# Kernel optimization log

Hardware: AMD Instinct MI355X
Metric: run time of the kernel (lower is better)

The kernel has to match this reference:

```python
import jax, jax.numpy as jnp
import numpy as np
from jax.scipy.special import gammaln

S, N, T = 8, 32, 262144
EPS = 1e-16  # emission clamp, as in torch .clamp(min=1e-16)


def setup_inputs() -> dict:
    key = jax.random.key(0)
    k1, k2, k3, k4 = jax.random.split(key, 4)
    spikes = jax.random.randint(k1, (T, N), 0, 2).astype(jnp.int32)  # binary counts
    convolved_spikes = 0.5 * jax.random.normal(k2, (T, N), dtype=jnp.float32)
    weight = 0.1 * jax.random.normal(k3, (S, N, N), dtype=jnp.float32)
    bias = 0.1 * jax.random.normal(k4, (N,), dtype=jnp.float32)
    eye = jnp.eye(S, dtype=jnp.float32)
    transition_matrix = eye * 0.98 + (0.02 / (S - 1)) * (1.0 - eye)
    return {"spikes": spikes, "convolved_spikes": convolved_spikes,
            "weight": weight, "bias": bias, "transition_matrix": transition_matrix}


def reference(spikes, convolved_spikes, weight, bias, transition_matrix):
    n_states = weight.shape[0]
    init_p = jnp.ones(n_states, dtype=convolved_spikes.dtype) / n_states
    A = transition_matrix  # (S, S)

    # firing_rates: sigmoid(bias + conv @ W[s].T) -> (S, T, N)
    rates = jax.nn.sigmoid(bias[None, None, :] +
                           jnp.einsum('tn,smn->stm', convolved_spikes, weight))
    x = spikes.astype(rates.dtype)
    # Poisson log-likelihood summed over neurons, then (S,T) -> (T,S)
    log_emission = (x[None] * jnp.log(rates) - rates - gammaln(x + 1.0)[None]).sum(-1).T

    emission = jnp.clip(jnp.exp(log_emission), EPS)  # (T, S)

    # forward pass (scaling)
    a0 = init_p * emission[0]
    c0 = a0.sum()
    a0 = a0 / c0

    def fstep(a_prev, em_t):
        a = em_t * (A.T @ a_prev)
        c = a.sum()
        an = a / c
        return an, (an, c)

    _, (alpha_rest, c_rest) = jax.lax.scan(fstep, a0, emission[1:])
    alpha = jnp.concatenate([a0[None], alpha_rest])  # (T, S)
    c = jnp.concatenate([c0[None], c_rest])          # (T,)

    # backward pass
    def bstep(b_next, ec):
        em_t1, c_t1 = ec
        b = A @ (b_next * em_t1) / c_t1
        return b, b

    b_last = jnp.ones(n_states, dtype=emission.dtype)
    _, beta_head = jax.lax.scan(bstep, b_last, (emission[1:], c[1:]), reverse=True)
    beta = jnp.concatenate([beta_head, b_last[None]])  # (T, S)

    gamma = alpha * beta  # (T, S)
    xi = (alpha[:-1, :, None] * emission[1:, None, :] *
          A[None, :, :] * beta[1:, None, :]) / c[1:, None, None]  # (T-1, S, S)
    return gamma, xi
```

## Files before the change

### kernel.cpp

```cpp
#include <hip/hip_runtime.h>
#include <math.h>


constexpr int TT  = 262144;
constexpr int LL  = 64;
constexpr int CK  = TT / LL;
constexpr int CPG = 16;
constexpr int NG  = CK / CPG;
constexpr int NSG = 16;
constexpr int EP  = 516;

typedef __attribute__((ext_vector_type(8))) short bf16x8;
typedef __attribute__((ext_vector_type(4))) float f32x4;

__device__ __forceinline__ float rcp_nr(float x) {
  float r = __builtin_amdgcn_rcpf(x);
  return r * (2.0f - x * r);
}
__device__ __forceinline__ unsigned short f2bf(float f) {
  unsigned u = __float_as_uint(f);
  u += 0x7FFFu + ((u >> 16) & 1u);
  return (unsigned short)(u >> 16);
}
__device__ __forceinline__ float bf2f(unsigned short h) {
  return __uint_as_float(((unsigned)h) << 16);
}

#define SWZ8(x, k) __int_as_float(__builtin_amdgcn_ds_swizzle(__float_as_int(x), (((k) << 5) | 0x18)))
#define SWZX(x, d) __int_as_float(__builtin_amdgcn_ds_swizzle(__float_as_int(x), (((d) << 10) | 0x1F)))
#define BPERM(a, x) __int_as_float(__builtin_amdgcn_ds_bpermute((a), __float_as_int(x)))

#define TREE8(dst, v) { float s01=v[0]+v[1], s23=v[2]+v[3], s45=v[4]+v[5], s67=v[6]+v[7]; dst = (s01+s23)+(s45+s67); }

__global__ __launch_bounds__(256) void k_emission(
    const int* __restrict__ spikes, const float* __restrict__ conv,
    const float* __restrict__ W, const float* __restrict__ bias,
    float* __restrict__ em, float* __restrict__ iemax) {
  __shared__ short sWbf[256 * 40];
  __shared__ unsigned sMask[64];
  const int tid = threadIdx.x;
  const int lane = tid & 63;
  const int wv = tid >> 6;
  const int T0 = blockIdx.x * 64;
  const int q = lane & 15;
  const int rg = lane >> 4;

#pragma unroll
  for (int it = 0; it < 8; ++it) {
    int idx4 = tid + it * 256;
    float4 w4 = ((const float4*)W)[idx4];
    int sm = idx4 >> 3, n0 = (idx4 & 7) << 2;
    ushort4 h;
    h.x = f2bf(w4.x); h.y = f2bf(w4.y); h.z = f2bf(w4.z); h.w = f2bf(w4.w);
    *(ushort4*)&sWbf[sm * 40 + n0] = h;
  }
#pragma unroll
  for (int it = 0; it < 8; ++it) {
    int idx = it * 256 + tid;
    int t = idx >> 5;
    int v = spikes[(size_t)(T0 + t) * 32 + (idx & 31)];
    unsigned long long b = __ballot(v != 0);
    if ((lane & 31) == 0) sMask[t] = (unsigned)(b >> (lane & 32));
  }
  __syncthreads();

  const int tg0 = T0 + wv * 16;
  const float* cp = conv + (size_t)(tg0 + q) * 32 + rg * 8;
  float4 ca = *(const float4*)cp;
  float4 cb = *(const float4*)(cp + 4);
  bf16x8 ch, cl;
  {
    float cv[8] = {ca.x, ca.y, ca.z, ca.w, cb.x, cb.y, cb.z, cb.w};
#pragma unroll
    for (int e2 = 0; e2 < 8; ++e2) {
      unsigned short hb = f2bf(cv[e2]);
      ch[e2] = (short)hb;
      cl[e2] = (short)f2bf(cv[e2] - bf2f(hb));
    }
  }
  const float4 bjlo = ((const float4*)bias)[rg];
  const float4 bjhi = ((const float4*)bias)[rg + 4];
  const unsigned mk = sMask[wv * 16 + q];
  constexpr float L2E = 1.4426950408889634f;
  const f32x4 zacc = {0.f, 0.f, 0.f, 0.f};

  float les[8];
#pragma unroll
  for (int s = 0; s < 8; ++s) {
    float part0 = 0.f, part1 = 0.f;
#pragma unroll
    for (int par = 0; par < 2; ++par) {
      const int tile = s * 2 + par;
      bf16x8 wf = *(bf16x8*)&sWbf[(tile * 16 + q) * 40 + rg * 8];
      f32x4 acc = __builtin_amdgcn_mfma_f32_16x16x32_bf16(wf, cl, zacc, 0, 0, 0);
      acc = __builtin_amdgcn_mfma_f32_16x16x32_bf16(wf, ch, acc, 0, 0, 0);
      const float4 bj = par ? bjhi : bjlo;
      float bja[4] = {bj.x, bj.y, bj.z, bj.w};
      float sumr = 0.f, pr = 1.f;
#pragma unroll
      for (int r = 0; r < 4; ++r) {
        float z = acc[r] + bja[r];
        float u = __builtin_amdgcn_exp2f(z * -L2E);
        float p = 1.f + u;
        sumr += __builtin_amdgcn_rcpf(p);
        int m = par * 16 + rg * 4 + r;
        pr *= ((mk >> m) & 1u) ? p : 1.f;
      }
      sumr += SWZX(sumr, 16); sumr += __shfl_xor(sumr, 32);
      pr   *= SWZX(pr, 16);   pr   *= __shfl_xor(pr, 32);
      float pt = fmaf(-L2E, sumr, -__builtin_amdgcn_logf(pr));
      if (par == 0) part0 = pt; else part1 = pt;
    }
    les[s] = part0 + part1;
  }
  float e[8];
#pragma unroll
  for (int s = 0; s < 8; ++s) e[s] = fmaxf(__builtin_amdgcn_exp2f(les[s]), 1e-16f);
  float mx = e[0];
#pragma unroll
  for (int s = 1; s < 8; ++s) mx = fmaxf(mx, e[s]);
  if (lane < 16) {
    float4 o0 = {e[0], e[1], e[2], e[3]};
    float4 o1 = {e[4], e[5], e[6], e[7]};
    *(float4*)&em[(size_t)(tg0 + q) * 8] = o0;
    *(float4*)&em[(size_t)(tg0 + q) * 8 + 4] = o1;
    iemax[tg0 + q] = rcp_nr(mx);
  }
}

__global__ __launch_bounds__(128) void k_fwd_chunks(
    const float* __restrict__ em, const float* __restrict__ iemax,
    const float* __restrict__ A, float* __restrict__ Pf,
    float* __restrict__ Gf) {
  __shared__ float sE[16 * EP];
  __shared__ float sM[16 * 64];
  const int tid = threadIdx.x;
  const int cl = tid >> 3, jc = tid & 7;
  const int c = blockIdx.x * 16 + cl;
  const float b_ = A[1];
  const float aa = A[0] - b_;

  for (int idx = tid; idx < 8192; idx += 128) {
    int gi = blockIdx.x * 8192 + idx;
    sE[(idx >> 9) * EP + (idx & 511)] = em[gi] * iemax[gi >> 3];
  }
  __syncthreads();

  float p[8];
#pragma unroll
  for (int k = 0; k < 8; ++k) p[k] = (k == jc) ? 1.f : 0.f;
  const float* eb = &sE[cl * EP];
  for (int t = 0; t < 64; ++t) {
    float4 e0 = *(const float4*)&eb[t * 8];
    float4 e1 = *(const float4*)&eb[t * 8 + 4];
    float e[8] = {e0.x, e0.y, e0.z, e0.w, e1.x, e1.y, e1.z, e1.w};
    if (c == 0 && t == 0) {
#pragma unroll
      for (int r = 0; r < 8; ++r) p[r] = e[r] * p[r];
    } else {
      float sg; TREE8(sg, p);
      float bs = b_ * sg;
#pragma unroll
      for (int r = 0; r < 8; ++r) p[r] = e[r] * fmaf(aa, p[r], bs);
    }
    if ((t & 7) == 7) {
      float m = p[0];
#pragma unroll
      for (int k = 1; k < 8; ++k) m = fmaxf(m, p[k]);
      m = fmaxf(m, SWZX(m, 1)); m = fmaxf(m, SWZX(m, 2)); m = fmaxf(m, SWZX(m, 4));
      float rm = __builtin_amdgcn_rcpf(m);
#pragma unroll
      for (int k = 0; k < 8; ++k) p[k] *= rm;
    }
  }
#pragma unroll
  for (int r = 0; r < 8; ++r) {
    sM[cl * 64 + r * 8 + jc] = p[r];
    Pf[(size_t)c * 64 + r * 8 + jc] = p[r];
  }
  __syncthreads();

  if (tid < 64) {
    const int L = tid;
    int ad[8];
#pragma unroll
    for (int k = 0; k < 8; ++k) ad[k] = (((k << 3) | (L & 7))) << 2;
    float S = sM[L];
    for (int m = 1; m < 16; ++m) {
      float4 r0 = *(const float4*)&sM[m * 64 + (L >> 3) * 8];
      float4 r1 = *(const float4*)&sM[m * 64 + (L >> 3) * 8 + 4];
      float acc;
      acc =      r0.x * BPERM(ad[0], S);
      acc = fmaf(r0.y,  BPERM(ad[1], S), acc);
      acc = fmaf(r0.z,  BPERM(ad[2], S), acc);
      acc = fmaf(r0.w,  BPERM(ad[3], S), acc);
      acc = fmaf(r1.x,  BPERM(ad[4], S), acc);
      acc = fmaf(r1.y,  BPERM(ad[5], S), acc);
      acc = fmaf(r1.z,  BPERM(ad[6], S), acc);
      acc = fmaf(r1.w,  BPERM(ad[7], S), acc);
      S = acc;
      if ((m & 3) == 3) {
        float mx = S;
        mx = fmaxf(mx, SWZX(mx, 1));  mx = fmaxf(mx, SWZX(mx, 2));
        mx = fmaxf(mx, SWZX(mx, 4));  mx = fmaxf(mx, SWZX(mx, 8));
        mx = fmaxf(mx, SWZX(mx, 16)); mx = fmaxf(mx, __shfl_xor(mx, 32));
        S *= __builtin_amdgcn_rcpf(mx);
      }
    }
    Gf[(size_t)blockIdx.x * 64 + L] = S;
  }
}

__global__ __launch_bounds__(1024) void k_fwd_mid(
    const float* __restrict__ Gf, float* __restrict__ vg) {
  __shared__ float sG[NG * 64];
  __shared__ float sgS[NSG * 64];
  __shared__ float sgE[NSG * 8];
  const int tid = threadIdx.x, wv = tid >> 6, L = tid & 63;
  for (int idx = tid; idx < NG * 64; idx += 1024) sG[idx] = Gf[idx];
  __syncthreads();

  int ad[8];
#pragma unroll
  for (int k = 0; k < 8; ++k) ad[k] = (((k << 3) | (L & 7))) << 2;
  const int ad2 = ((L & 7) * 9) << 2;

  {
    float S = sG[wv * 1024 + L];
    for (int m = 1; m < 16; ++m) {
      const float* mb = &sG[(wv * 16 + m) * 64 + (L >> 3) * 8];
      float4 r0 = *(const float4*)mb;
      float4 r1 = *(const float4*)(mb + 4);
      float acc;
      acc =      r0.x * BPERM(ad[0], S);
      acc = fmaf(r0.y,  BPERM(ad[1], S), acc);
      acc = fmaf(r0.z,  BPERM(ad[2], S), acc);
      acc = fmaf(r0.w,  BPERM(ad[3], S), acc);
      acc = fmaf(r1.x,  BPERM(ad[4], S), acc);
      acc = fmaf(r1.y,  BPERM(ad[5], S), acc);
      acc = fmaf(r1.z,  BPERM(ad[6], S), acc);
      acc = fmaf(r1.w,  BPERM(ad[7], S), acc);
      S = acc;
      if ((m & 3) == 3) {
        float mx = S;
        mx = fmaxf(mx, SWZX(mx, 1));  mx = fmaxf(mx, SWZX(mx, 2));
        mx = fmaxf(mx, SWZX(mx, 4));  mx = fmaxf(mx, SWZX(mx, 8));
        mx = fmaxf(mx, SWZX(mx, 16)); mx = fmaxf(mx, __shfl_xor(mx, 32));
        S *= __builtin_amdgcn_rcpf(mx);
      }
    }
    sgS[wv * 64 + L] = S;
  }
  __syncthreads();

  if (wv == 0) {
    float vj = 0.125f;
    for (int sg = 0; sg < 16; ++sg) {
      if (L < 8) sgE[sg * 8 + L] = vj;
      float t = sgS[sg * 64 + L] * vj;
      t += SWZX(t, 1); t += SWZX(t, 2); t += SWZX(t, 4);
      float t2 = t + SWZX(t, 8); t2 += SWZX(t2, 16); t2 += __shfl_xor(t2, 32);
      vj = BPERM(ad2, t) * rcp_nr(t2);
    }
  }
  __syncthreads();

  {
    float vj = sgE[wv * 8 + (L & 7)];
    for (int gl = 0; gl < 16; ++gl) {
      int g = wv * 16 + gl;
      if (L < 8) vg[g * 8 + L] = vj;
      float t = sG[g * 64 + L] * vj;
      t += SWZX(t, 1); t += SWZX(t, 2); t += SWZX(t, 4);
      float t2 = t + SWZX(t, 8); t2 += SWZX(t2, 16); t2 += __shfl_xor(t2, 32);
      vj = BPERM(ad2, t) * rcp_nr(t2);
    }
  }
}

__global__ __launch_bounds__(128) void k_fwd_replay(
    const float* __restrict__ em, const float* __restrict__ A,
    const float* __restrict__ Pf, const float* __restrict__ vg,
    float* __restrict__ bf, float* __restrict__ alpha,
    float* __restrict__ cvec) {
  __shared__ float sE[16 * EP];
  __shared__ float sBf[16 * 8];
  const int tid = threadIdx.x;
  const int cl = tid >> 3, jl = tid & 7;
  const int c = blockIdx.x * 16 + cl;
  const float b_ = A[1];
  const float aa = A[0] - b_;

  for (int idx = tid; idx < 8192; idx += 128)
    sE[(idx >> 9) * EP + (idx & 511)] = em[(size_t)blockIdx.x * 8192 + idx];

  if (tid < 64) {
    const int L = tid;
    const int ad2 = ((L & 7) * 9) << 2;
    float f[16];
#pragma unroll
    for (int m = 0; m < 16; ++m) f[m] = Pf[(size_t)(blockIdx.x * 16 + m) * 64 + L];
    float vj = vg[blockIdx.x * 8 + (L & 7)];
#pragma unroll
    for (int m = 0; m < 16; ++m) {
      if (L < 8) {
        sBf[m * 8 + L] = vj;
        bf[(size_t)(blockIdx.x * 16 + m) * 8 + L] = vj;
      }
      float t = f[m] * vj;
      t += SWZX(t, 1); t += SWZX(t, 2); t += SWZX(t, 4);
      float t2 = t + SWZX(t, 8); t2 += SWZX(t2, 16); t2 += __shfl_xor(t2, 32);
      vj = BPERM(ad2, t) * rcp_nr(t2);
    }
  }
  __syncthreads();

  float u[8];
#pragma unroll
  for (int k = 0; k < 8; ++k) u[k] = sBf[cl * 8 + k];
  float rs = 1.f;
  const float* eb = &sE[cl * EP];
  for (int t = 0; t < 64; ++t) {
    float4 e0 = *(const float4*)&eb[t * 8];
    float4 e1 = *(const float4*)&eb[t * 8 + 4];
    float e[8] = {e0.x, e0.y, e0.z, e0.w, e1.x, e1.y, e1.z, e1.w};
    float un[8];
    if (c == 0 && t == 0) {
#pragma unroll
      for (int r = 0; r < 8; ++r) un[r] = 0.125f * e[r];
    } else {
      float sg; TREE8(sg, u);
      float bs = b_ * sg;
#pragma unroll
      for (int r = 0; r < 8; ++r) un[r] = (e[r] * rs) * fmaf(aa, u[r], bs);
    }
    float s; TREE8(s, un);
    float rsn = rcp_nr(s);
    float myu = un[0];
#pragma unroll
    for (int k = 1; k < 8; ++k) myu = (jl == k) ? un[k] : myu;
    int tg = c * 64 + t;
    alpha[(size_t)tg * 8 + jl] = myu * rsn;
    if (jl == 0) cvec[tg] = s;
#pragma unroll
    for (int k = 0; k < 8; ++k) u[k] = un[k];
    rs = rsn;
  }
}

__global__ __launch_bounds__(128) void k_bwd_chunks(
    const float* __restrict__ em, const float* __restrict__ cvec,
    const float* __restrict__ A, float* __restrict__ Rb,
    float* __restrict__ Gb) {
  __shared__ float sS[16 * EP];
  __shared__ float sM[16 * 64];
  const int tid = threadIdx.x;
  const int cl = tid >> 3, il = tid & 7;
  const int c = blockIdx.x * 16 + cl;
  const float b_ = A[1];
  const float aa = A[0] - b_;

  for (int idx = tid; idx < 8192; idx += 128) {
    int gi = blockIdx.x * 8192 + idx;
    sS[(idx >> 9) * EP + (idx & 511)] = em[gi] * rcp_nr(cvec[gi >> 3]);
  }
  __syncthreads();

  float rv[8];
#pragma unroll
  for (int k = 0; k < 8; ++k) rv[k] = (k == il) ? 1.f : 0.f;
  const float* db = &sS[cl * EP];
  for (int t = 0; t < 64; ++t) {
    float4 d0 = *(const float4*)&db[t * 8];
    float4 d1 = *(const float4*)&db[t * 8 + 4];
    float d[8] = {d0.x, d0.y, d0.z, d0.w, d1.x, d1.y, d1.z, d1.w};
    float sg; TREE8(sg, rv);
    float bs = b_ * sg;
#pragma unroll
    for (int j = 0; j < 8; ++j) rv[j] = fmaf(aa, rv[j], bs) * d[j];
  }
  {
    float4 o0 = {rv[0], rv[1], rv[2], rv[3]};
    float4 o1 = {rv[4], rv[5], rv[6], rv[7]};
    *(float4*)&sM[cl * 64 + il * 8] = o0;
    *(float4*)&sM[cl * 64 + il * 8 + 4] = o1;
    *(float4*)&Rb[(size_t)c * 64 + il * 8] = o0;
    *(float4*)&Rb[(size_t)c * 64 + il * 8 + 4] = o1;
  }
  __syncthreads();

  if (tid < 64) {
    const int L = tid;
    float S = sM[L];
    for (int m = 1; m < 16; ++m) {
      const float* mb = &sM[m * 64 + (L & 7)];
      float acc;
      acc =      SWZ8(S, 0) * mb[0];
      acc = fmaf(SWZ8(S, 1), mb[8],  acc);
      acc = fmaf(SWZ8(S, 2), mb[16], acc);
      acc = fmaf(SWZ8(S, 3), mb[24], acc);
      acc = fmaf(SWZ8(S, 4), mb[32], acc);
      acc = fmaf(SWZ8(S, 5), mb[40], acc);
      acc = fmaf(SWZ8(S, 6), mb[48], acc);
      acc = fmaf(SWZ8(S, 7), mb[56], acc);
      S = acc;
    }
    Gb[(size_t)blockIdx.x * 64 + L] = S;
  }
}

__global__ __launch_bounds__(1024) void k_bwd_mid(
    const float* __restrict__ Gb, float* __restrict__ wg) {
  __shared__ float sG[NG * 64];
  __shared__ float sgS[NSG * 64];
  __shared__ float sgE[NSG * 8];
  const int tid = threadIdx.x, wv = tid >> 6, L = tid & 63;
  for (int idx = tid; idx < NG * 64; idx += 1024) sG[idx] = Gb[idx];
  __syncthreads();

  const int ad2 = ((L & 7) * 9) << 2;
  {
    float S = sG[wv * 1024 + L];
    for (int m = 1; m < 16; ++m) {
      const float* mb = &sG[(wv * 16 + m) * 64 + (L & 7)];
      float acc;
      acc =      SWZ8(S, 0) * mb[0];
      acc = fmaf(SWZ8(S, 1), mb[8],  acc);
      acc = fmaf(SWZ8(S, 2), mb[16], acc);
      acc = fmaf(SWZ8(S, 3), mb[24], acc);
      acc = fmaf(SWZ8(S, 4), mb[32], acc);
      acc = fmaf(SWZ8(S, 5), mb[40], acc);
      acc = fmaf(SWZ8(S, 6), mb[48], acc);
      acc = fmaf(SWZ8(S, 7), mb[56], acc);
      S = acc;
    }
    sgS[wv * 64 + L] = S;
  }
  __syncthreads();

  if (wv == 0) {
    float wj = 1.f;
    for (int sg = 15; sg >= 0; --sg) {
      if (L < 8) sgE[sg * 8 + L] = wj;
      float t = sgS[sg * 64 + L] * wj;
      t += SWZX(t, 1); t += SWZX(t, 2); t += SWZX(t, 4);
      wj = BPERM(ad2, t);
    }
  }
  __syncthreads();

  {
    float wj = sgE[wv * 8 + (L & 7)];
    for (int gl = 15; gl >= 0; --gl) {
      int g = wv * 16 + gl;
      if (L < 8) wg[g * 8 + L] = wj;
      float t = sG[g * 64 + L] * wj;
      t += SWZX(t, 1); t += SWZX(t, 2); t += SWZX(t, 4);
      wj = BPERM(ad2, t);
    }
  }
}

__global__ __launch_bounds__(1024) void k_bwd_replay(
    const float* __restrict__ em, const float* __restrict__ cvec,
    const float* __restrict__ A, const float* __restrict__ bf,
    const float* __restrict__ wg, const float* __restrict__ Rb,
    float* __restrict__ gamma, float* __restrict__ xi) {
  __shared__ float sQ[16 * 512];
  __shared__ float sAl[16 * 512];
  __shared__ float sGb[16 * 8];
  const int tid = threadIdx.x, wv = tid >> 6, L = tid & 63;
  const int i = L >> 3, j = L & 7;
  const int c = blockIdx.x * 16 + wv;
  const float Aij = A[i * 8 + j];

  for (int idx = tid; idx < 8192; idx += 1024) {
    int gi = blockIdx.x * 8192 + idx;
    sQ[idx] = em[gi] * rcp_nr(cvec[gi >> 3]);
    int cl2 = idx >> 9, rr = (idx >> 3) & 63, s = idx & 7;
    float av;
    if (rr == 0) av = bf[(blockIdx.x * 16 + cl2) * 8 + s];
    else av = gamma[((size_t)(blockIdx.x * 16 + cl2) * 64 + rr - 1) * 8 + s];
    sAl[idx] = av;
  }
  if (wv == 0) {
    const int ad2 = ((L & 7) * 9) << 2;
    float f[16];
#pragma unroll
    for (int m = 0; m < 16; ++m) f[m] = Rb[(size_t)(blockIdx.x * 16 + m) * 64 + L];
    float vj = wg[blockIdx.x * 8 + (L & 7)];
#pragma unroll
    for (int m = 15; m >= 0; --m) {
      if (L < 8) sGb[m * 8 + L] = vj;
      float t = f[m] * vj;
      t += SWZX(t, 1); t += SWZX(t, 2); t += SWZX(t, 4);
      vj = BPERM(ad2, t);
    }
  }
  __syncthreads();

  float b = sGb[wv * 8 + j];
  {
    int te = c * 64 + 63;
    if (L < 8) {
      float al = gamma[(size_t)te * 8 + L];
      gamma[(size_t)te * 8 + L] = al * b;
    }
  }
  for (int t = 63; t >= 0; --t) {
    int tg = c * 64 + t;
    float q = sQ[wv * 512 + t * 8 + j] * b;
    float apv = sAl[wv * 512 + t * 8 + i];
    if (tg > 0) xi[(size_t)(tg - 1) * 64 + L] = apv * Aij * q;
    float p = Aij * q;
    p += SWZX(p, 1); p += SWZX(p, 2); p += SWZX(p, 4);
    if (t > 0 && j == 0) gamma[(size_t)(tg - 1) * 8 + i] = apv * p;
    b = __shfl(p, (L & 7) * 8);
  }
}

extern "C" void kernel_launch(void* const* d_in, const int* in_sizes, int n_in,
                              void* d_out, int out_size, void* d_ws, size_t ws_size,
                              hipStream_t stream) {
  const int*   spikes = (const int*)  d_in[0];
  const float* conv   = (const float*)d_in[1];
  const float* W      = (const float*)d_in[2];
  const float* bias   = (const float*)d_in[3];
  const float* A      = (const float*)d_in[4];

  float* out   = (float*)d_out;
  float* gamma = out;
  float* xi    = out + (size_t)TT * 8;

  float* ws    = (float*)d_ws;
  float* em    = ws;
  float* iemax = em + (size_t)TT * 8;
  float* cvec  = iemax + TT;
  float* Pf    = cvec + TT;
  float* Rb    = Pf;
  float* Gf    = Pf + (size_t)CK * 64;
  float* Gb    = Gf;
  float* vg    = Gf + NG * 64;
  float* wg    = vg + NG * 8;
  float* bf    = wg + NG * 8;
  (void)in_sizes; (void)n_in; (void)out_size; (void)ws_size;

  k_emission  <<<TT / 64, 256, 0, stream>>>(spikes, conv, W, bias, em, iemax);
  k_fwd_chunks<<<NG, 128, 0, stream>>>(em, iemax, A, Pf, Gf);
  k_fwd_mid   <<<1, 1024, 0, stream>>>(Gf, vg);
  k_fwd_replay<<<NG, 128, 0, stream>>>(em, A, Pf, vg, bf, gamma, cvec);
  k_bwd_chunks<<<NG, 128, 0, stream>>>(em, cvec, A, Rb, Gb);
  k_bwd_mid   <<<1, 1024, 0, stream>>>(Gb, wg);
  k_bwd_replay<<<NG, 1024, 0, stream>>>(em, cvec, A, bf, wg, Rb, gamma, xi);
}
```

Before: 143.3 us.

## Fuse forward replay with backward chunk pass and restructure emission MFMA loop

Merges the forward replay kernel and the backward chunk-transfer kernel into one launch. It reuses the emission tile already in shared memory and keeps the per-step reciprocal scaling constants in LDS, so emissions and cvec are not reloaded from global memory. The emission kernel now preloads all 16 weight fragments and interleaves the two MFMA tiles per state with a single cross-lane reduction. Several recurrence loops gain unroll pragmas. The costs are one fewer launch and less global traffic, paid for with more LDS per block and higher register pressure from the preloaded fragments.

```diff
diff --git a/kernel.cpp b/kernel.cpp
--- a/kernel.cpp
+++ b/kernel.cpp
@@ -78,47 +78,48 @@
       cl[e2] = (short)f2bf(cv[e2] - bf2f(hb));
     }
   }
-  const float4 bjlo = ((const float4*)bias)[rg];
-  const float4 bjhi = ((const float4*)bias)[rg + 4];
+  const float4 bl4 = ((const float4*)bias)[rg];
+  const float4 bh4 = ((const float4*)bias)[rg + 4];
+  const float bjlo[4] = {bl4.x, bl4.y, bl4.z, bl4.w};
+  const float bjhi[4] = {bh4.x, bh4.y, bh4.z, bh4.w};
   const unsigned mk = sMask[wv * 16 + q];
   constexpr float L2E = 1.4426950408889634f;
   const f32x4 zacc = {0.f, 0.f, 0.f, 0.f};
 
-  float les[8];
-#pragma unroll
-  for (int s = 0; s < 8; ++s) {
-    float part0 = 0.f, part1 = 0.f;
-#pragma unroll
-    for (int par = 0; par < 2; ++par) {
-      const int tile = s * 2 + par;
-      bf16x8 wf = *(bf16x8*)&sWbf[(tile * 16 + q) * 40 + rg * 8];
-      f32x4 acc = __builtin_amdgcn_mfma_f32_16x16x32_bf16(wf, cl, zacc, 0, 0, 0);
-      acc = __builtin_amdgcn_mfma_f32_16x16x32_bf16(wf, ch, acc, 0, 0, 0);
-      const float4 bj = par ? bjhi : bjlo;
-      float bja[4] = {bj.x, bj.y, bj.z, bj.w};
-      float sumr = 0.f, pr = 1.f;
-#pragma unroll
-      for (int r = 0; r < 4; ++r) {
-        float z = acc[r] + bja[r];
-        float u = __builtin_amdgcn_exp2f(z * -L2E);
-        float p = 1.f + u;
-        sumr += __builtin_amdgcn_rcpf(p);
-        int m = par * 16 + rg * 4 + r;
-        pr *= ((mk >> m) & 1u) ? p : 1.f;
-      }
-      sumr += SWZX(sumr, 16); sumr += __shfl_xor(sumr, 32);
-      pr   *= SWZX(pr, 16);   pr   *= __shfl_xor(pr, 32);
-      float pt = fmaf(-L2E, sumr, -__builtin_amdgcn_logf(pr));
-      if (par == 0) part0 = pt; else part1 = pt;
-    }
-    les[s] = part0 + part1;
-  }
+  bf16x8 wfr[16];
+#pragma unroll
+  for (int t16 = 0; t16 < 16; ++t16)
+    wfr[t16] = *(bf16x8*)&sWbf[(t16 * 16 + q) * 40 + rg * 8];
+
   float e[8];
-#pragma unroll
-  for (int s = 0; s < 8; ++s) e[s] = fmaxf(__builtin_amdgcn_exp2f(les[s]), 1e-16f);
-  float mx = e[0];
-#pragma unroll
-  for (int s = 1; s < 8; ++s) mx = fmaxf(mx, e[s]);
+  float mx = 0.f;
+#pragma unroll
+  for (int sp = 0; sp < 8; ++sp) {
+    f32x4 a0 = __builtin_amdgcn_mfma_f32_16x16x32_bf16(wfr[2 * sp], cl, zacc, 0, 0, 0);
+    a0 = __builtin_amdgcn_mfma_f32_16x16x32_bf16(wfr[2 * sp], ch, a0, 0, 0, 0);
+    f32x4 a1 = __builtin_amdgcn_mfma_f32_16x16x32_bf16(wfr[2 * sp + 1], cl, zacc, 0, 0, 0);
+    a1 = __builtin_amdgcn_mfma_f32_16x16x32_bf16(wfr[2 * sp + 1], ch, a1, 0, 0, 0);
+    float sumr = 0.f, pr = 1.f;
+#pragma unroll
+    for (int r = 0; r < 4; ++r) {
+      float z0 = a0[r] + bjlo[r];
+      float u0 = __builtin_amdgcn_exp2f(z0 * -L2E);
+      float p0 = 1.f + u0;
+      sumr += __builtin_amdgcn_rcpf(p0);
+      pr *= ((mk >> (rg * 4 + r)) & 1u) ? p0 : 1.f;
+      float z1 = a1[r] + bjhi[r];
+      float u1 = __builtin_amdgcn_exp2f(z1 * -L2E);
+      float p1 = 1.f + u1;
+      sumr += __builtin_amdgcn_rcpf(p1);
+      pr *= ((mk >> (16 + rg * 4 + r)) & 1u) ? p1 : 1.f;
+    }
+    float g = fmaf(-L2E, sumr, -__builtin_amdgcn_logf(pr));
+    g += SWZX(g, 16);
+    g += __shfl_xor(g, 32);
+    float ev = fmaxf(__builtin_amdgcn_exp2f(g), 1e-16f);
+    e[sp] = ev;
+    mx = fmaxf(mx, ev);
+  }
   if (lane < 16) {
     float4 o0 = {e[0], e[1], e[2], e[3]};
     float4 o1 = {e[4], e[5], e[6], e[7]};
@@ -150,6 +151,7 @@
 #pragma unroll
   for (int k = 0; k < 8; ++k) p[k] = (k == jc) ? 1.f : 0.f;
   const float* eb = &sE[cl * EP];
+#pragma unroll 8
   for (int t = 0; t < 64; ++t) {
     float4 e0 = *(const float4*)&eb[t * 8];
     float4 e1 = *(const float4*)&eb[t * 8 + 4];
@@ -278,13 +280,15 @@
   }
 }
 
-__global__ __launch_bounds__(128) void k_fwd_replay(
+__global__ __launch_bounds__(128) void k_frbc(
     const float* __restrict__ em, const float* __restrict__ A,
-    const float* __restrict__ Pf, const float* __restrict__ vg,
-    float* __restrict__ bf, float* __restrict__ alpha,
-    float* __restrict__ cvec) {
+    const float* __restrict__ vg, float* __restrict__ bf,
+    float* __restrict__ alpha, float* __restrict__ cvec,
+    float* __restrict__ PfRb, float* __restrict__ Gb) {
   __shared__ float sE[16 * EP];
+  __shared__ float sRC[16 * 66];
   __shared__ float sBf[16 * 8];
+  __shared__ float sM[16 * 64];
   const int tid = threadIdx.x;
   const int cl = tid >> 3, jl = tid & 7;
   const int c = blockIdx.x * 16 + cl;
@@ -299,7 +303,7 @@
     const int ad2 = ((L & 7) * 9) << 2;
     float f[16];
 #pragma unroll
-    for (int m = 0; m < 16; ++m) f[m] = Pf[(size_t)(blockIdx.x * 16 + m) * 64 + L];
+    for (int m = 0; m < 16; ++m) f[m] = PfRb[(size_t)(blockIdx.x * 16 + m) * 64 + L];
     float vj = vg[blockIdx.x * 8 + (L & 7)];
 #pragma unroll
     for (int m = 0; m < 16; ++m) {
@@ -315,77 +319,66 @@
   }
   __syncthreads();
 
-  float u[8];
-#pragma unroll
-  for (int k = 0; k < 8; ++k) u[k] = sBf[cl * 8 + k];
-  float rs = 1.f;
-  const float* eb = &sE[cl * EP];
-  for (int t = 0; t < 64; ++t) {
-    float4 e0 = *(const float4*)&eb[t * 8];
-    float4 e1 = *(const float4*)&eb[t * 8 + 4];
-    float e[8] = {e0.x, e0.y, e0.z, e0.w, e1.x, e1.y, e1.z, e1.w};
-    float un[8];
-    if (c == 0 && t == 0) {
-#pragma unroll
-      for (int r = 0; r < 8; ++r) un[r] = 0.125f * e[r];
-    } else {
-      float sg; TREE8(sg, u);
+  {
+    float u[8];
+#pragma unroll
+    for (int k = 0; k < 8; ++k) u[k] = sBf[cl * 8 + k];
+    float rs = 1.f;
+    const float* eb = &sE[cl * EP];
+#pragma unroll 4
+    for (int t = 0; t < 64; ++t) {
+      float4 e0 = *(const float4*)&eb[t * 8];
+      float4 e1 = *(const float4*)&eb[t * 8 + 4];
+      float e[8] = {e0.x, e0.y, e0.z, e0.w, e1.x, e1.y, e1.z, e1.w};
+      float un[8];
+      if (c == 0 && t == 0) {
+#pragma unroll
+        for (int r = 0; r < 8; ++r) un[r] = 0.125f * e[r];
+      } else {
+        float sg; TREE8(sg, u);
+        float bs = b_ * sg;
+#pragma unroll
+        for (int r = 0; r < 8; ++r) un[r] = (e[r] * rs) * fmaf(aa, u[r], bs);
+      }
+      float s; TREE8(s, un);
+      float rsn = rcp_nr(s);
+      float myu = un[0];
+#pragma unroll
+      for (int k = 1; k < 8; ++k) myu = (jl == k) ? un[k] : myu;
+      int tg = c * 64 + t;
+      alpha[(size_t)tg * 8 + jl] = myu * rsn;
+      if (jl == 0) { cvec[tg] = s; sRC[cl * 66 + t] = rsn; }
+#pragma unroll
+      for (int k = 0; k < 8; ++k) u[k] = un[k];
+      rs = rsn;
+    }
+  }
+  __syncthreads();
+
+  {
+    float rv[8];
+#pragma unroll
+    for (int k = 0; k < 8; ++k) rv[k] = (k == jl) ? 1.f : 0.f;
+    const float* eb = &sE[cl * EP];
+    const float* rb = &sRC[cl * 66];
+#pragma unroll 4
+    for (int t = 0; t < 64; ++t) {
+      float rc = rb[t];
+      float4 d0 = *(const float4*)&eb[t * 8];
+      float4 d1 = *(const float4*)&eb[t * 8 + 4];
+      float d[8] = {d0.x * rc, d0.y * rc, d0.z * rc, d0.w * rc,
+                    d1.x * rc, d1.y * rc, d1.z * rc, d1.w * rc};
+      float sg; TREE8(sg, rv);
       float bs = b_ * sg;
 #pragma unroll
-      for (int r = 0; r < 8; ++r) un[r] = (e[r] * rs) * fmaf(aa, u[r], bs);
-    }
-    float s; TREE8(s, un);
-    float rsn = rcp_nr(s);
-    float myu = un[0];
-#pragma unroll
-    for (int k = 1; k < 8; ++k) myu = (jl == k) ? un[k] : myu;
-    int tg = c * 64 + t;
-    alpha[(size_t)tg * 8 + jl] = myu * rsn;
-    if (jl == 0) cvec[tg] = s;
-#pragma unroll
-    for (int k = 0; k < 8; ++k) u[k] = un[k];
-    rs = rsn;
-  }
-}
-
-__global__ __launch_bounds__(128) void k_bwd_chunks(
-    const float* __restrict__ em, const float* __restrict__ cvec,
-    const float* __restrict__ A, float* __restrict__ Rb,
-    float* __restrict__ Gb) {
-  __shared__ float sS[16 * EP];
-  __shared__ float sM[16 * 64];
-  const int tid = threadIdx.x;
-  const int cl = tid >> 3, il = tid & 7;
-  const int c = blockIdx.x * 16 + cl;
-  const float b_ = A[1];
-  const float aa = A[0] - b_;
-
-  for (int idx = tid; idx < 8192; idx += 128) {
-    int gi = blockIdx.x * 8192 + idx;
-    sS[(idx >> 9) * EP + (idx & 511)] = em[gi] * rcp_nr(cvec[gi >> 3]);
-  }
-  __syncthreads();
-
-  float rv[8];
-#pragma unroll
-  for (int k = 0; k < 8; ++k) rv[k] = (k == il) ? 1.f : 0.f;
-  const float* db = &sS[cl * EP];
-  for (int t = 0; t < 64; ++t) {
-    float4 d0 = *(const float4*)&db[t * 8];
-    float4 d1 = *(const float4*)&db[t * 8 + 4];
-    float d[8] = {d0.x, d0.y, d0.z, d0.w, d1.x, d1.y, d1.z, d1.w};
-    float sg; TREE8(sg, rv);
-    float bs = b_ * sg;
-#pragma unroll
-    for (int j = 0; j < 8; ++j) rv[j] = fmaf(aa, rv[j], bs) * d[j];
-  }
-  {
+      for (int j = 0; j < 8; ++j) rv[j] = fmaf(aa, rv[j], bs) * d[j];
+    }
     float4 o0 = {rv[0], rv[1], rv[2], rv[3]};
     float4 o1 = {rv[4], rv[5], rv[6], rv[7]};
-    *(float4*)&sM[cl * 64 + il * 8] = o0;
-    *(float4*)&sM[cl * 64 + il * 8 + 4] = o1;
-    *(float4*)&Rb[(size_t)c * 64 + il * 8] = o0;
-    *(float4*)&Rb[(size_t)c * 64 + il * 8 + 4] = o1;
+    *(float4*)&sM[cl * 64 + jl * 8] = o0;
+    *(float4*)&sM[cl * 64 + jl * 8 + 4] = o1;
+    *(float4*)&PfRb[(size_t)c * 64 + jl * 8] = o0;
+    *(float4*)&PfRb[(size_t)c * 64 + jl * 8 + 4] = o1;
   }
   __syncthreads();
 
@@ -507,6 +500,7 @@
       gamma[(size_t)te * 8 + L] = al * b;
     }
   }
+#pragma unroll 4
   for (int t = 63; t >= 0; --t) {
     int tg = c * 64 + t;
     float q = sQ[wv * 512 + t * 8 + j] * b;
@@ -548,8 +542,7 @@
   k_emission  <<<TT / 64, 256, 0, stream>>>(spikes, conv, W, bias, em, iemax);
   k_fwd_chunks<<<NG, 128, 0, stream>>>(em, iemax, A, Pf, Gf);
   k_fwd_mid   <<<1, 1024, 0, stream>>>(Gf, vg);
-  k_fwd_replay<<<NG, 128, 0, stream>>>(em, A, Pf, vg, bf, gamma, cvec);
-  k_bwd_chunks<<<NG, 128, 0, stream>>>(em, cvec, A, Rb, Gb);
+  k_frbc      <<<NG, 128, 0, stream>>>(em, A, vg, bf, gamma, cvec, Pf, Gb);
   k_bwd_mid   <<<1, 1024, 0, stream>>>(Gb, wg);
   k_bwd_replay<<<NG, 1024, 0, stream>>>(em, cvec, A, bf, wg, Rb, gamma, xi);
 }
```

Measured after the change: 126.5 us. 1.13x faster.
